# Kernel tuning notes

Hardware: AMD Instinct MI355X
Metric: run time of the kernel (lower is better)

## Reference

```python
import jax, jax.numpy as jnp
import numpy as np

N = 6144  # number of collocation points == number of RBF centers


def setup_inputs() -> dict:
    key = jax.random.key(0)
    ks = jax.random.split(key, 8)
    f = lambda k, s: jax.random.normal(k, s, dtype=jnp.float32)
    return {
        "x": f(ks[0], (N, 1)),
        "z": f(ks[1], (N, 1)),
        "t": f(ks[2], (N, 1)),
        "c": f(ks[3], (N, 3)),
        "v1": f(ks[4], (1, N)),
        "v2": f(ks[5], (1, N)),
        "v3": f(ks[6], (1, N)),
        "v4": f(ks[7], (1, N)),
    }


def _forward(x, z, t, c, v1, v2, v3, v4):
    def ff(xi, zi, ti):
        pts = jnp.concatenate([xi, zi, ti], axis=1)        # [N, 3]
        d = c[None, :, :] - pts[:, None, :]                # [N, M, 3]
        G = jnp.exp(-0.5 * jnp.sum(d * d, axis=2))         # [N, M] Gaussian Gram matrix
        p = G @ v1.T                                        # [N, 1]
        b = G @ v2.T
        u = G @ v3.T
        w = G @ v4.T
        return (p, b, u, w)

    # first + second directional derivatives w.r.t. x (nested forward-mode JVP,
    # mirroring the nested tf.autodiff.ForwardAccumulator structure)
    def d1x(xx):
        return jax.jvp(lambda a: ff(a, z, t), (xx,), (jnp.ones_like(xx),))[1]

    (dpdx, dbdx, dudx, dwdx), (_, d2bd2x, d2ud2x, d2wd2x) = jax.jvp(
        d1x, (x,), (jnp.ones_like(x),))

    # first + second derivatives w.r.t. z
    def d1z(zz):
        return jax.jvp(lambda a: ff(x, a, t), (zz,), (jnp.ones_like(zz),))[1]

    (dpdz, dbdz, dudz, dwdz), (_, d2bd2z, d2ud2z, d2wd2z) = jax.jvp(
        d1z, (z,), (jnp.ones_like(z),))

    # first derivatives w.r.t. t only
    _, (dpdt, dbdt, dudt, dwdt) = jax.jvp(
        lambda a: ff(x, z, a), (t,), (jnp.ones_like(t),))

    return (dudx, dudz, dudt, dwdx, dwdz, dwdt,
            dbdx, dbdz, dbdt, dpdx, dpdz,
            d2ud2x, d2ud2z, d2wd2x, d2wd2z, d2bd2x, d2bd2z)


def reference(x, z, t, c, v1, v2, v3, v4):
    return _forward(x, z, t, c, v1, v2, v3, v4)
```

## Files before the change

kernel.cpp:

```cpp
#include <hip/hip_runtime.h>
#include <hip/hip_bf16.h>


#define NPTS 6144
#define SPLIT 8
#define KC (NPTS / SPLIT)
#define NSTEP (KC / 32)
#define VROW 776
#define S2  0.7213475204444817f
#define L2E 1.4426950408889634f

typedef float  f32x4  __attribute__((ext_vector_type(4)));
typedef float  f32x2  __attribute__((ext_vector_type(2)));
typedef __bf16 bf16x8 __attribute__((ext_vector_type(8)));

#if defined(__has_builtin) && __has_builtin(__builtin_amdgcn_exp2f)
#define EXP2F(x) __builtin_amdgcn_exp2f(x)
#else
#define EXP2F(x) __expf((x) * 0.6931471805599453f)
#endif

__global__ __launch_bounds__(256) void rbf_fused(
    const float* __restrict__ xp, const float* __restrict__ zp,
    const float* __restrict__ tp, const float* __restrict__ cp,
    const float* __restrict__ v1p, const float* __restrict__ v2p,
    const float* __restrict__ v3p, const float* __restrict__ v4p,
    float* __restrict__ out) {
  __shared__ __align__(16) float  cs[3][KC];
  __shared__ __align__(16) __bf16 vlds[21][VROW];

  const int rg = blockIdx.x % 96;
  const int s  = blockIdx.x / 96;

  for (int j = threadIdx.x; j < KC; j += 256) {
    const int jg = s * KC + j;
    const float cx = cp[3 * jg], cz = cp[3 * jg + 1], ct = cp[3 * jg + 2];
    cs[0][j] = cx * L2E; cs[1][j] = cz * L2E; cs[2][j] = ct * L2E;
    const float aj  = S2 * fmaf(cx, cx, fmaf(cz, cz, ct * ct));
    const float e2a = EXP2F(-aj);
    const float a1 = v1p[jg] * e2a;
    vlds[0][j] = (__bf16)a1;
    vlds[1][j] = (__bf16)(cx * a1);
    vlds[2][j] = (__bf16)(cz * a1);
    const float vs[3] = {v2p[jg] * e2a, v3p[jg] * e2a, v4p[jg] * e2a};
#pragma unroll
    for (int k2 = 0; k2 < 3; ++k2) {
      const float v = vs[k2];
      const int r = 3 + 6 * k2;
      vlds[r + 0][j] = (__bf16)v;
      vlds[r + 1][j] = (__bf16)(cx * v);
      vlds[r + 2][j] = (__bf16)(cz * v);
      vlds[r + 3][j] = (__bf16)(ct * v);
      vlds[r + 4][j] = (__bf16)(cx * cx * v);
      vlds[r + 5][j] = (__bf16)(cz * cz * v);
    }
  }
  __syncthreads();

  const int w    = threadIdx.x >> 6;
  const int lane = threadIdx.x & 63;
  const int lo   = lane & 15;
  const int hi   = lane >> 4;
  const int lo5  = lo % 5;

  const int rowbase = rg * 64 + w * 16;
  const int row = rowbase + lo;
  const float xi = xp[row], zi = zp[row], ti = tp[row];
  const f32x2 xs2 = {xi, xi}, zs2 = {zi, zi}, ts2 = {ti, ti};

  f32x4 acc0 = {0.f, 0.f, 0.f, 0.f};
  f32x4 acc1 = {0.f, 0.f, 0.f, 0.f};

#pragma unroll 2
  for (int step = 0; step < NSTEP; ++step) {
    const int kb = hi * 8 + step * 32;
    const f32x2* cxp = (const f32x2*)&cs[0][kb];
    const f32x2* czp = (const f32x2*)&cs[1][kb];
    const f32x2* ctp = (const f32x2*)&cs[2][kb];
    const bf16x8 b0 = *(const bf16x8*)&vlds[lo][kb];
    const bf16x8 b1 = *(const bf16x8*)&vlds[16 + lo5][kb];

    bf16x8 af;
#pragma unroll
    for (int i = 0; i < 4; ++i) {
      const f32x2 d = __builtin_elementwise_fma(
          cxp[i], xs2,
          __builtin_elementwise_fma(czp[i], zs2, ctp[i] * ts2));
      af[2 * i]     = (__bf16)EXP2F(d.x);
      af[2 * i + 1] = (__bf16)EXP2F(d.y);
    }
    acc0 = __builtin_amdgcn_mfma_f32_16x16x32_bf16(af, b0, acc0, 0, 0, 0);
    acc1 = __builtin_amdgcn_mfma_f32_16x16x32_bf16(af, b1, acc1, 0, 0, 0);
  }

  __syncthreads();
  float* redw = reinterpret_cast<float*>(vlds) + w * (16 * 33);
#pragma unroll
  for (int reg = 0; reg < 4; ++reg) {
    const int r = hi * 4 + reg;
    redw[r * 33 + lo]      = acc0[reg];
    redw[r * 33 + lo + 16] = acc1[reg];
  }
  __syncthreads();

  if (lane < 16) {
    const int orow = rowbase + lane;
    float wv[21];
#pragma unroll
    for (int c = 0; c < 21; ++c) wv[c] = redw[lane * 33 + c];
    const float x = xp[orow], z = zp[orow], t = tp[orow];
    const float gi = EXP2F(-S2 * fmaf(x, x, fmaf(z, z, t * t)));
    const float x2 = fmaf(x, x, -1.f), z2 = fmaf(z, z, -1.f);
    float* o = out;
    atomicAdd(&o[0 * NPTS + orow],  gi * (wv[10] - x * wv[9]));
    atomicAdd(&o[1 * NPTS + orow],  gi * (wv[11] - z * wv[9]));
    atomicAdd(&o[2 * NPTS + orow],  gi * (wv[12] - t * wv[9]));
    atomicAdd(&o[3 * NPTS + orow],  gi * (wv[16] - x * wv[15]));
    atomicAdd(&o[4 * NPTS + orow],  gi * (wv[17] - z * wv[15]));
    atomicAdd(&o[5 * NPTS + orow],  gi * (wv[18] - t * wv[15]));
    atomicAdd(&o[6 * NPTS + orow],  gi * (wv[4]  - x * wv[3]));
    atomicAdd(&o[7 * NPTS + orow],  gi * (wv[5]  - z * wv[3]));
    atomicAdd(&o[8 * NPTS + orow],  gi * (wv[6]  - t * wv[3]));
    atomicAdd(&o[9 * NPTS + orow],  gi * (wv[1]  - x * wv[0]));
    atomicAdd(&o[10 * NPTS + orow], gi * (wv[2]  - z * wv[0]));
    atomicAdd(&o[11 * NPTS + orow], gi * (wv[13] - 2.f * x * wv[10] + x2 * wv[9]));
    atomicAdd(&o[12 * NPTS + orow], gi * (wv[14] - 2.f * z * wv[11] + z2 * wv[9]));
    atomicAdd(&o[13 * NPTS + orow], gi * (wv[19] - 2.f * x * wv[16] + x2 * wv[15]));
    atomicAdd(&o[14 * NPTS + orow], gi * (wv[20] - 2.f * z * wv[17] + z2 * wv[15]));
    atomicAdd(&o[15 * NPTS + orow], gi * (wv[7]  - 2.f * x * wv[4]  + x2 * wv[3]));
    atomicAdd(&o[16 * NPTS + orow], gi * (wv[8]  - 2.f * z * wv[5]  + z2 * wv[3]));
  }
}

extern "C" void kernel_launch(void* const* d_in, const int* in_sizes, int n_in,
                              void* d_out, int out_size, void* d_ws, size_t ws_size,
                              hipStream_t stream) {
  const float* xp  = (const float*)d_in[0];
  const float* zp  = (const float*)d_in[1];
  const float* tp  = (const float*)d_in[2];
  const float* cp  = (const float*)d_in[3];
  const float* v1p = (const float*)d_in[4];
  const float* v2p = (const float*)d_in[5];
  const float* v3p = (const float*)d_in[6];
  const float* v4p = (const float*)d_in[7];

  rbf_fused<<<96 * SPLIT, 256, 0, stream>>>(xp, zp, tp, cp,
                                            v1p, v2p, v3p, v4p, (float*)d_out);
}
```

Before: 77.58 us.

## Replace atomic split-K reduction with workspace partials and separate epilogue kernel

The main kernel now writes each split's 21 partial sums per row into a workspace instead of doing 17 atomicAdds per row per split into the output. A second small kernel sums the 8 splits, applies the Gaussian epilogue and writes the outputs directly. This removes atomic contention and the need for the output to be pre-zeroed, at the cost of an extra kernel launch and about 4 MB of workspace traffic. The epilogue runs only 96 blocks of 64 threads, so it may be latency-bound.

```diff
diff --git a/kernel.cpp b/kernel.cpp
--- a/kernel.cpp
+++ b/kernel.cpp
@@ -25,7 +25,7 @@
     const float* __restrict__ tp, const float* __restrict__ cp,
     const float* __restrict__ v1p, const float* __restrict__ v2p,
     const float* __restrict__ v3p, const float* __restrict__ v4p,
-    float* __restrict__ out) {
+    float* __restrict__ ws) {
   __shared__ __align__(16) float  cs[3][KC];
   __shared__ __align__(16) __bf16 vlds[21][VROW];
 
@@ -94,7 +94,8 @@
   }
 
   __syncthreads();
-  float* redw = reinterpret_cast<float*>(vlds) + w * (16 * 33);
+  float* redbase = reinterpret_cast<float*>(vlds);
+  float* redw = redbase + w * (16 * 33);
 #pragma unroll
   for (int reg = 0; reg < 4; ++reg) {
     const int r = hi * 4 + reg;
@@ -103,33 +104,50 @@
   }
   __syncthreads();
 
-  if (lane < 16) {
-    const int orow = rowbase + lane;
-    float wv[21];
+  float* wsp = ws + (size_t)s * 21 * NPTS + rg * 64;
+  for (int idx = threadIdx.x; idx < 21 * 64; idx += 256) {
+    const int c = idx >> 6, r = idx & 63;
+    wsp[c * NPTS + r] = redbase[(r >> 4) * (16 * 33) + (r & 15) * 33 + c];
+  }
+}
+
+__global__ __launch_bounds__(64) void rbf_epilogue(
+    const float* __restrict__ xp, const float* __restrict__ zp,
+    const float* __restrict__ tp, const float* __restrict__ ws,
+    float* __restrict__ out) {
+  const int row = blockIdx.x * 64 + threadIdx.x;
+
+  float wv[21];
 #pragma unroll
-    for (int c = 0; c < 21; ++c) wv[c] = redw[lane * 33 + c];
-    const float x = xp[orow], z = zp[orow], t = tp[orow];
-    const float gi = EXP2F(-S2 * fmaf(x, x, fmaf(z, z, t * t)));
-    const float x2 = fmaf(x, x, -1.f), z2 = fmaf(z, z, -1.f);
-    float* o = out;
-    atomicAdd(&o[0 * NPTS + orow],  gi * (wv[10] - x * wv[9]));
-    atomicAdd(&o[1 * NPTS + orow],  gi * (wv[11] - z * wv[9]));
-    atomicAdd(&o[2 * NPTS + orow],  gi * (wv[12] - t * wv[9]));
-    atomicAdd(&o[3 * NPTS + orow],  gi * (wv[16] - x * wv[15]));
-    atomicAdd(&o[4 * NPTS + orow],  gi * (wv[17] - z * wv[15]));
-    atomicAdd(&o[5 * NPTS + orow],  gi * (wv[18] - t * wv[15]));
-    atomicAdd(&o[6 * NPTS + orow],  gi * (wv[4]  - x * wv[3]));
-    atomicAdd(&o[7 * NPTS + orow],  gi * (wv[5]  - z * wv[3]));
-    atomicAdd(&o[8 * NPTS + orow],  gi * (wv[6]  - t * wv[3]));
-    atomicAdd(&o[9 * NPTS + orow],  gi * (wv[1]  - x * wv[0]));
-    atomicAdd(&o[10 * NPTS + orow], gi * (wv[2]  - z * wv[0]));
-    atomicAdd(&o[11 * NPTS + orow], gi * (wv[13] - 2.f * x * wv[10] + x2 * wv[9]));
-    atomicAdd(&o[12 * NPTS + orow], gi * (wv[14] - 2.f * z * wv[11] + z2 * wv[9]));
-    atomicAdd(&o[13 * NPTS + orow], gi * (wv[19] - 2.f * x * wv[16] + x2 * wv[15]));
-    atomicAdd(&o[14 * NPTS + orow], gi * (wv[20] - 2.f * z * wv[17] + z2 * wv[15]));
-    atomicAdd(&o[15 * NPTS + orow], gi * (wv[7]  - 2.f * x * wv[4]  + x2 * wv[3]));
-    atomicAdd(&o[16 * NPTS + orow], gi * (wv[8]  - 2.f * z * wv[5]  + z2 * wv[3]));
+  for (int c = 0; c < 21; ++c) wv[c] = ws[c * NPTS + row];
+#pragma unroll
+  for (int s = 1; s < SPLIT; ++s) {
+    const float* p = ws + (size_t)s * 21 * NPTS + row;
+#pragma unroll
+    for (int c = 0; c < 21; ++c) wv[c] += p[c * NPTS];
   }
+
+  const float x = xp[row], z = zp[row], t = tp[row];
+  const float gi = EXP2F(-S2 * fmaf(x, x, fmaf(z, z, t * t)));
+  const float x2 = fmaf(x, x, -1.f), z2 = fmaf(z, z, -1.f);
+  float* o = out;
+  o[0 * NPTS + row]  = gi * (wv[10] - x * wv[9]);
+  o[1 * NPTS + row]  = gi * (wv[11] - z * wv[9]);
+  o[2 * NPTS + row]  = gi * (wv[12] - t * wv[9]);
+  o[3 * NPTS + row]  = gi * (wv[16] - x * wv[15]);
+  o[4 * NPTS + row]  = gi * (wv[17] - z * wv[15]);
+  o[5 * NPTS + row]  = gi * (wv[18] - t * wv[15]);
+  o[6 * NPTS + row]  = gi * (wv[4]  - x * wv[3]);
+  o[7 * NPTS + row]  = gi * (wv[5]  - z * wv[3]);
+  o[8 * NPTS + row]  = gi * (wv[6]  - t * wv[3]);
+  o[9 * NPTS + row]  = gi * (wv[1]  - x * wv[0]);
+  o[10 * NPTS + row] = gi * (wv[2]  - z * wv[0]);
+  o[11 * NPTS + row] = gi * (wv[13] - 2.f * x * wv[10] + x2 * wv[9]);
+  o[12 * NPTS + row] = gi * (wv[14] - 2.f * z * wv[11] + z2 * wv[9]);
+  o[13 * NPTS + row] = gi * (wv[19] - 2.f * x * wv[16] + x2 * wv[15]);
+  o[14 * NPTS + row] = gi * (wv[20] - 2.f * z * wv[17] + z2 * wv[15]);
+  o[15 * NPTS + row] = gi * (wv[7]  - 2.f * x * wv[4]  + x2 * wv[3]);
+  o[16 * NPTS + row] = gi * (wv[8]  - 2.f * z * wv[5]  + z2 * wv[3]);
 }
 
 extern "C" void kernel_launch(void* const* d_in, const int* in_sizes, int n_in,
@@ -143,7 +161,9 @@
   const float* v2p = (const float*)d_in[5];
   const float* v3p = (const float*)d_in[6];
   const float* v4p = (const float*)d_in[7];
+  float* ws = (float*)d_ws;
 
   rbf_fused<<<96 * SPLIT, 256, 0, stream>>>(xp, zp, tp, cp,
-                                            v1p, v2p, v3p, v4p, (float*)d_out);
+                                            v1p, v2p, v3p, v4p, ws);
+  rbf_epilogue<<<96, 64, 0, stream>>>(xp, zp, tp, ws, (float*)d_out);
 }
```

After: 113.0 us. 45.7% more time.
